# Performance work log

Hardware: AMD Instinct MI355X
Metric: run time of the kernel (lower is better)

The kernel has to match this reference:

```python
import jax, jax.numpy as jnp
import numpy as np

N_USERS = 100000
N_ITEMS = 50000
DIM = 64
HID = 64
E = 3200000
B = 16384


def setup_inputs() -> dict:
    key = jax.random.key(0)
    ks = jax.random.split(key, 16)
    N = N_USERS + N_ITEMS
    return {
        "users": jax.random.randint(ks[0], (B,), 0, N_USERS),
        "items": jax.random.randint(ks[1], (B,), 0, N_ITEMS),
        "edge_index": jax.random.randint(ks[2], (2, E), 0, N),
        "edge_weight": jax.random.uniform(ks[3], (E,), dtype=jnp.float32),
        # learned parameters
        "U": jax.random.normal(ks[4], (N_USERS, DIM), jnp.float32) * 0.1,
        "I": jax.random.normal(ks[5], (N_ITEMS, DIM), jnp.float32) * 0.1,
        "W0": jax.random.normal(ks[6], (DIM, HID), jnp.float32) / np.sqrt(DIM),
        "b0": jnp.zeros((HID,), jnp.float32),
        "g0": jnp.ones((HID,), jnp.float32),
        "be0": jnp.zeros((HID,), jnp.float32),
        "W1": jax.random.normal(ks[7], (HID, HID), jnp.float32) / np.sqrt(HID),
        "b1": jnp.zeros((HID,), jnp.float32),
        "g1": jnp.ones((HID,), jnp.float32),
        "be1": jnp.zeros((HID,), jnp.float32),
        "Wp": jax.random.normal(ks[8], (HID, DIM), jnp.float32) / np.sqrt(HID),
        "bp": jnp.zeros((DIM,), jnp.float32),
        "bu": jnp.zeros((N_USERS,), jnp.float32),
        "bi": jnp.zeros((N_ITEMS,), jnp.float32),
        "mu": jnp.zeros((), jnp.float32),
    }


def _layernorm(h, g, b, eps=1e-5):
    m = jnp.mean(h, axis=-1, keepdims=True)
    v = jnp.mean(jnp.square(h - m), axis=-1, keepdims=True)
    return (h - m) * jax.lax.rsqrt(v + eps) * g + b


def reference(users, items, edge_index, edge_weight, U, I,
              W0, b0, g0, be0, W1, b1, g1, be1, Wp, bp, bu, bi, mu):
    N = U.shape[0] + I.shape[0]
    x = jnp.concatenate([U, I], axis=0)  # [N, DIM]

    # GCN normalization with added self-loops (torch_geometric gcn_norm)
    loop = jnp.arange(N)
    src = jnp.concatenate([edge_index[0], loop])
    dst = jnp.concatenate([edge_index[1], loop])
    ew = jnp.concatenate([edge_weight, jnp.ones((N,), edge_weight.dtype)])
    deg = jax.ops.segment_sum(ew, dst, num_segments=N)
    dinv = jnp.where(deg > 0, jax.lax.rsqrt(deg), 0.0)
    norm = dinv[src] * ew * dinv[dst]  # [E+N]

    def conv(h, W, b):
        hw = h @ W  # [N, HID]
        msgs = norm[:, None] * hw[src]  # gather: [E+N, HID]
        return jax.ops.segment_sum(msgs, dst, num_segments=N) + b

    # layer 0: conv -> layernorm -> relu -> (dropout=identity, eval) -> residual
    h = x
    h_in = h
    h = conv(h, W0, b0)
    h = jax.nn.relu(_layernorm(h, g0, be0)) + h_in
    # layer 1
    h_in = h
    h = conv(h, W1, b1)
    h = jax.nn.relu(_layernorm(h, g1, be1)) + h_in

    h = h @ Wp + bp  # proj_out: [N, DIM]
    h_user = h[:U.shape[0]]
    h_item = h[U.shape[0]:]

    s = jnp.sum(h_user[users] * h_item[items], axis=-1)
    s = s + bu[users] + bi[items] + mu
    return jnp.clip(s, 1.0, 5.0)
```

## Files before the change

### kernel.cpp

```cpp
#include <hip/hip_runtime.h>

#define NU 100000
#define NI 50000
#define NN 150000
#define D  64
#define CAP 47
#define OVF_MAX 4096

#define BINSHIFT 8
#define BINW 256
#define NBINS 586
#define BINCAP 5848
#define STAGE_CAP 12
#define EPT 4
#define SPILL_CAP 262144
#define BIN_BLOCKS 768
#define GEMM_BLOCKS 2048

typedef unsigned int uint;
typedef unsigned short ushort;

__device__ __forceinline__ float half_reduce_add(float v) {
    #pragma unroll
    for (int m = 16; m >= 1; m >>= 1) v += __shfl_xor(v, m, 64);
    return v;
}
__device__ __forceinline__ ushort f2bf(float f) {
    union { float f; uint i; } c; c.f = f;
    uint r = c.i + 0x7FFF + ((c.i >> 16) & 1);
    return (ushort)(r >> 16);
}
__device__ __forceinline__ float lane_bcast(float v, int l) {
    return __int_as_float(__builtin_amdgcn_readlane(__float_as_int(v), l));
}
__device__ __forceinline__ uint enc14(float w) {
    uint b = __float_as_uint(w) + 0x00020000u;
    return b & 0xFFFC0000u;
}
__device__ __forceinline__ float dec14(uint r) {
    return __uint_as_float(r & 0xFFFC0000u);
}
__device__ __forceinline__ void spill_one(int d, uint s, float w,
        uint2* __restrict__ spill, int* __restrict__ spillcnt) {
    int si = atomicAdd(spillcnt, 1);
    if (si < SPILL_CAP) spill[si] = make_uint2(s | enc14(w), (uint)d);
}

__global__ __launch_bounds__(256) void k_bin_gemm(
        const int* __restrict__ src, const int* __restrict__ dst,
        const float* __restrict__ ew, int* __restrict__ bincur,
        uint2* __restrict__ binbuf, uint2* __restrict__ spill,
        int* __restrict__ spillcnt, int E,
        const float* __restrict__ U, const float* __restrict__ I,
        const float* __restrict__ W0, ushort* __restrict__ hw2b) {
    __shared__ uint2 stage[NBINS][STAGE_CAP];
    __shared__ int scnt[NBINS];
    if (blockIdx.x >= BIN_BLOCKS) {
        int lane = threadIdx.x & 63;
        float wreg[64];
        #pragma unroll
        for (int k = 0; k < 64; ++k) wreg[k] = W0[k * 64 + lane];
        int wid = (blockIdx.x - BIN_BLOCKS) * 4 + (threadIdx.x >> 6);
        int tw = GEMM_BLOCKS * 4;
        for (int n = wid; n < NN; n += tw) {
            float xv = (n < NU) ? U[(size_t)n * D + lane]
                                : I[(size_t)(n - NU) * D + lane];
            float a0 = 0.f, a1 = 0.f, a2 = 0.f, a3 = 0.f;
            #pragma unroll
            for (int k = 0; k < 64; k += 4) {
                a0 = fmaf(lane_bcast(xv, k + 0), wreg[k + 0], a0);
                a1 = fmaf(lane_bcast(xv, k + 1), wreg[k + 1], a1);
                a2 = fmaf(lane_bcast(xv, k + 2), wreg[k + 2], a2);
                a3 = fmaf(lane_bcast(xv, k + 3), wreg[k + 3], a3);
            }
            hw2b[(size_t)n * D + lane] = f2bf((a0 + a1) + (a2 + a3));
        }
        return;
    }
    int t = threadIdx.x;
    for (int i = t; i < NBINS; i += 256) scnt[i] = 0;
    __syncthreads();
    const int batch = 256 * EPT;
    for (int base = blockIdx.x * batch; base < E; base += BIN_BLOCKS * batch) {
        int dd[EPT]; uint ss[EPT]; float ww[EPT]; int ok[EPT];
        #pragma unroll
        for (int k = 0; k < EPT; ++k) {
            int e = base + k * 256 + t;
            ok[k] = (e < E);
            if (ok[k]) { dd[k] = dst[e]; ss[k] = (uint)src[e]; ww[k] = ew[e]; }
        }
        #pragma unroll
        for (int k = 0; k < EPT; ++k) {
            if (!ok[k]) continue;
            int bin = dd[k] >> BINSHIFT;
            int slot = atomicAdd(&scnt[bin], 1);
            if (slot < STAGE_CAP) {
                stage[bin][slot] = make_uint2(
                    ss[k] | ((uint)(dd[k] & (BINW - 1)) << 18),
                    (uint)__float_as_int(ww[k]));
            } else {
                spill_one(dd[k], ss[k], ww[k], spill, spillcnt);
            }
        }
        __syncthreads();
        for (int bin = t; bin < NBINS; bin += 256) {
            int c = scnt[bin]; if (c > STAGE_CAP) c = STAGE_CAP;
            while (c >= 8) {
                int b0 = atomicAdd(&bincur[bin], 8);
                if (b0 + 8 <= BINCAP) {
                    uint4* o4 = (uint4*)(binbuf + (size_t)bin * BINCAP + b0);
                    uint2* s2 = &stage[bin][c - 8];
                    o4[0] = make_uint4(s2[0].x, s2[0].y, s2[1].x, s2[1].y);
                    o4[1] = make_uint4(s2[2].x, s2[2].y, s2[3].x, s2[3].y);
                    o4[2] = make_uint4(s2[4].x, s2[4].y, s2[5].x, s2[5].y);
                    o4[3] = make_uint4(s2[6].x, s2[6].y, s2[7].x, s2[7].y);
                } else {
                    for (int j = 0; j < 8; ++j) {
                        uint2 r = stage[bin][c - 8 + j];
                        spill_one((bin << BINSHIFT) + (int)(r.x >> 18),
                                  r.x & 0x3FFFFu, __int_as_float((int)r.y),
                                  spill, spillcnt);
                    }
                }
                c -= 8;
            }
            scnt[bin] = c;
        }
        __syncthreads();
    }
    for (int bin = t; bin < NBINS; bin += 256) {
        int c = scnt[bin]; if (c > STAGE_CAP) c = STAGE_CAP;
        if (c > 0) {
            int b0 = atomicAdd(&bincur[bin], c);
            for (int j = 0; j < c; ++j) {
                uint2 r = stage[bin][j];
                if (b0 + j < BINCAP) binbuf[(size_t)bin * BINCAP + b0 + j] = r;
                else spill_one((bin << BINSHIFT) + (int)(r.x >> 18),
                               r.x & 0x3FFFFu, __int_as_float((int)r.y),
                               spill, spillcnt);
            }
        }
    }
}

__global__ __launch_bounds__(256) void k_regroup(
        const int* __restrict__ bincur, const uint2* __restrict__ binbuf,
        const uint2* __restrict__ spill, const int* __restrict__ spillcnt,
        uint* __restrict__ recs, int* __restrict__ cursor,
        float* __restrict__ dinv, int4* __restrict__ ovf,
        int* __restrict__ ovfcnt, ushort* __restrict__ hw2b) {
    __shared__ uint image[256 * CAP];
    __shared__ int cnt[256];
    __shared__ float ovfw[256];
    int t = threadIdx.x;
    int bin = blockIdx.x;
    cnt[t] = 0; ovfw[t] = 0.0f;
    __syncthreads();
    int dbase = bin << BINSHIFT;
    int nrec = bincur[bin]; if (nrec > BINCAP) nrec = BINCAP;
    const uint2* bb = binbuf + (size_t)bin * BINCAP;
    for (int i = t; i < nrec; i += 256) {
        uint2 r = bb[i];
        int dl = (int)(r.x >> 18);
        int slot = atomicAdd(&cnt[dl], 1);
        uint s = r.x & 0x3FFFFu;
        float w = __int_as_float((int)r.y);
        if (slot < CAP) image[dl * CAP + slot] = enc14(w) | s;
        else {
            atomicAdd(&ovfw[dl], w);
            int o = atomicAdd(ovfcnt, 1);
            if (o < OVF_MAX)
                ovf[o] = make_int4(dbase + dl, (int)s, __float_as_int(w), 0);
        }
    }
    int ns = spillcnt[0]; if (ns > SPILL_CAP) ns = SPILL_CAP;
    for (int i = t; i < ns; i += 256) {
        uint2 e = spill[i];
        int d = (int)e.y;
        if (d < dbase || d >= dbase + BINW) continue;
        int dl = d - dbase;
        int slot = atomicAdd(&cnt[dl], 1);
        if (slot < CAP) image[dl * CAP + slot] = e.x;
        else {
            float w = dec14(e.x);
            atomicAdd(&ovfw[dl], w);
            int o = atomicAdd(ovfcnt, 1);
            if (o < OVF_MAX) ovf[o] = make_int4(d, (int)(e.x & 0x3FFFFu),
                                                __float_as_int(w), 0);
        }
    }
    __syncthreads();
    int ndl = NN - dbase; if (ndl > 256) ndl = 256;
    if (ndl <= 0) return;
    if (t < ndl) {
        int c = cnt[t];
        cursor[dbase + t] = c;
        if (c > CAP) c = CAP;
        float dg = ovfw[t];
        for (int j = 0; j < c; ++j) dg += dec14(image[t * CAP + j]);
        float dv = rsqrtf(dg + 1.0f);
        dinv[dbase + t] = dv;
        ovfw[t] = dv;
    }
    int tot = ndl * CAP;
    uint* out = recs + (size_t)dbase * CAP;
    for (int i = t; i < tot; i += 256) out[i] = image[i];
    __syncthreads();
    uint* hw = (uint*)hw2b + (size_t)dbase * 32;
    int tot32 = ndl * 32;
    for (int i = t; i < tot32; i += 256) {
        float di = ovfw[i >> 5];
        uint v = hw[i];
        uint lo = (uint)f2bf(__uint_as_float(v << 16) * di);
        uint hi = (uint)f2bf(__uint_as_float(v & 0xFFFF0000u) * di);
        hw[i] = lo | (hi << 16);
    }
}

__device__ __forceinline__ float2 conv_accum2(int n, int lane,
        const uint* __restrict__ hw2p, const int* __restrict__ cursor,
        const uint* __restrict__ recs, const int4* __restrict__ ovf,
        const int* __restrict__ ovfcnt) {
    int cnt = __builtin_amdgcn_readfirstlane(cursor[n]);
    if (cnt > CAP) cnt = CAP;
    uint rv = (lane < cnt) ? recs[(size_t)n * CAP + lane] : 0u;
    const int  vodd4 = (lane >> 5) << 2;
    const uint lb4   = (uint)(lane & 31) << 2;
    uint xs = *(const uint*)((const char*)hw2p + (((uint)n << 7) + lb4));
    float ax = 0.f, ay = 0.f;
    int cp = (cnt + 7) & ~7;

#define CA_DECL(c) uint x##c##0, x##c##1, x##c##2, x##c##3, \
                        w##c##0, w##c##1, w##c##2, w##c##3;
#define CA_GET(c, i, P) { \
    uint r = (uint)__builtin_amdgcn_ds_bpermute(vodd4 + 8 * (P), (int)rv); \
    w##c##i = r & 0xFFFC0000u; \
    x##c##i = *(const uint*)((const char*)hw2p + \
                             (((r & 0x3FFFFu) << 7) + lb4)); }
#define CA_ISSUE(c, P0) { CA_GET(c, 0, (P0)+0) CA_GET(c, 1, (P0)+1) \
                          CA_GET(c, 2, (P0)+2) CA_GET(c, 3, (P0)+3) }
#define CA_FMA1(c, i) { \
    ax = fmaf(__uint_as_float(w##c##i), __uint_as_float(x##c##i << 16), ax); \
    ay = fmaf(__uint_as_float(w##c##i), \
              __uint_as_float(x##c##i & 0xFFFF0000u), ay); }
#define CA_FMA(c) { CA_FMA1(c,0) CA_FMA1(c,1) CA_FMA1(c,2) CA_FMA1(c,3) }

    CA_DECL(A) CA_DECL(B) CA_DECL(G)
    if (cp > 0)  CA_ISSUE(A, 0)
    if (cp > 8)  CA_ISSUE(B, 4)
    if (cp > 16) CA_ISSUE(G, 8)
    if (cp > 0)  CA_FMA(A)
    if (cp > 24) CA_ISSUE(A, 12)
    if (cp > 8)  CA_FMA(B)
    if (cp > 32) CA_ISSUE(B, 16)
    if (cp > 16) CA_FMA(G)
    if (cp > 40) CA_ISSUE(G, 20)
    if (cp > 24) CA_FMA(A)
    if (cp > 32) CA_FMA(B)
    if (cp > 40) CA_FMA(G)
#undef CA_FMA
#undef CA_FMA1
#undef CA_ISSUE
#undef CA_GET
#undef CA_DECL

    ax += __shfl_xor(ax, 32, 64);
    ay += __shfl_xor(ay, 32, 64);
    ax += __uint_as_float(xs << 16);
    ay += __uint_as_float(xs & 0xFFFF0000u);
    int novf = __builtin_amdgcn_readfirstlane(ovfcnt[0]);
    if (novf > 0) {
        if (novf > OVF_MAX) novf = OVF_MAX;
        for (int j = 0; j < novf; ++j) {
            int4 e = ovf[j];
            if (e.x == n) {
                float w = __int_as_float(e.z);
                uint x = hw2p[(size_t)e.y * 32 + (lane & 31)];
                ax = fmaf(w, __int_as_float((int)(x << 16)), ax);
                ay = fmaf(w, __int_as_float((int)(x & 0xFFFF0000u)), ay);
            }
        }
    }
    return make_float2(ax, ay);
}

__device__ __forceinline__ float2 ln_relu2(float2 a, float di, int p,
        const float* __restrict__ b, const float* __restrict__ g,
        const float* __restrict__ be) {
    float2 bb = ((const float2*)b)[p];
    float v0 = fmaf(a.x, di, bb.x);
    float v1 = fmaf(a.y, di, bb.y);
    float m = half_reduce_add(v0 + v1) * (1.0f / 64.0f);
    float d0 = v0 - m, d1 = v1 - m;
    float var = half_reduce_add(d0 * d0 + d1 * d1) * (1.0f / 64.0f);
    float rs = rsqrtf(var + 1e-5f);
    float2 gg = ((const float2*)g)[p];
    float2 ee = ((const float2*)be)[p];
    return make_float2(fmaxf(fmaf(d0 * rs, gg.x, ee.x), 0.0f),
                       fmaxf(fmaf(d1 * rs, gg.y, ee.y), 0.0f));
}

__global__ __launch_bounds__(256) void k_conv1(
        const uint* __restrict__ hw2p, const int* __restrict__ cursor,
        const uint* __restrict__ recs, const int4* __restrict__ ovf,
        const int* __restrict__ ovfcnt, const float* __restrict__ dinv,
        const float* __restrict__ b, const float* __restrict__ g,
        const float* __restrict__ be, const float* __restrict__ U,
        const float* __restrict__ I, uint* __restrict__ out1) {
    int lane = threadIdx.x & 63;
    int n = __builtin_amdgcn_readfirstlane(blockIdx.x * 4 + (threadIdx.x >> 6));
    if (n >= NN) return;
    float2 a = conv_accum2(n, lane, hw2p, cursor, recs, ovf, ovfcnt);
    int p = lane & 31;
    float2 y = ln_relu2(a, dinv[n], p, b, g, be);
    const float* R = (n < NU) ? (U + (size_t)n * D) : (I + (size_t)(n - NU) * D);
    float2 rr = ((const float2*)R)[p];
    if (lane < 32) {
        out1[(size_t)n * 32 + p] =
            (uint)f2bf(y.x + rr.x) | ((uint)f2bf(y.y + rr.y) << 16);
    }
}

__global__ __launch_bounds__(256) void k_gemm2(
        const ushort* __restrict__ hb, const float* __restrict__ W,
        const float* __restrict__ dinv, ushort* __restrict__ out) {
    int lane = threadIdx.x & 63;
    float wreg[64];
    #pragma unroll
    for (int k = 0; k < 64; ++k) wreg[k] = W[k * 64 + lane];
    int wpb = blockDim.x >> 6;
    int wid = blockIdx.x * wpb + (threadIdx.x >> 6);
    int tw = gridDim.x * wpb;
    for (int n = wid; n < NN; n += tw) {
        float xv = __uint_as_float((uint)hb[(size_t)n * D + lane] << 16);
        float a0 = 0.f, a1 = 0.f, a2 = 0.f, a3 = 0.f;
        #pragma unroll
        for (int k = 0; k < 64; k += 4) {
            a0 = fmaf(lane_bcast(xv, k + 0), wreg[k + 0], a0);
            a1 = fmaf(lane_bcast(xv, k + 1), wreg[k + 1], a1);
            a2 = fmaf(lane_bcast(xv, k + 2), wreg[k + 2], a2);
            a3 = fmaf(lane_bcast(xv, k + 3), wreg[k + 3], a3);
        }
        out[(size_t)n * D + lane] = f2bf(((a0 + a1) + (a2 + a3)) * dinv[n]);
    }
}

__global__ __launch_bounds__(256) void k_conv2score(
        const uint* __restrict__ hw2p, const int* __restrict__ cursor,
        const uint* __restrict__ recs, const int4* __restrict__ ovf,
        const int* __restrict__ ovfcnt, const float* __restrict__ dinv,
        const float* __restrict__ b, const float* __restrict__ g,
        const float* __restrict__ be, const int* __restrict__ users,
        const int* __restrict__ items, const uint* __restrict__ h1b,
        const float* __restrict__ Wp, const float* __restrict__ bp,
        const float* __restrict__ bu, const float* __restrict__ bi,
        const float* __restrict__ mu, float* __restrict__ out, int B) {
    int lane = threadIdx.x & 63;
    float wreg[64];
    #pragma unroll
    for (int k = 0; k < 64; ++k) wreg[k] = Wp[k * 64 + lane];
    float bpl = bp[lane];
    int q = lane & 31;
    int wpb = blockDim.x >> 6;
    int wid = blockIdx.x * wpb + (threadIdx.x >> 6);
    int tw = gridDim.x * wpb;
    for (int p = wid; p < B; p += tw) {
        int un = users[p];
        int in = NU + items[p];
        int nu = __builtin_amdgcn_readfirstlane(un);
        float2 au = conv_accum2(nu, lane, hw2p, cursor, recs, ovf, ovfcnt);
        float2 yu = ln_relu2(au, dinv[nu], q, b, g, be);
        uint xu = h1b[(size_t)nu * 32 + q];
        float2 hu = make_float2(yu.x + __uint_as_float(xu << 16),
                                yu.y + __uint_as_float(xu & 0xFFFF0000u));
        int ni = __builtin_amdgcn_readfirstlane(in);
        float2 ai = conv_accum2(ni, lane, hw2p, cursor, recs, ovf, ovfcnt);
        float2 yi = ln_relu2(ai, dinv[ni], q, b, g, be);
        uint xi = h1b[(size_t)ni * 32 + q];
        float2 hi = make_float2(yi.x + __uint_as_float(xi << 16),
                                yi.y + __uint_as_float(xi & 0xFFFF0000u));
        float pu = bpl, pi = bpl;
        #pragma unroll
        for (int j = 0; j < 32; ++j) {
            pu = fmaf(lane_bcast(hu.x, j), wreg[2 * j], pu);
            pu = fmaf(lane_bcast(hu.y, j), wreg[2 * j + 1], pu);
            pi = fmaf(lane_bcast(hi.x, j), wreg[2 * j], pi);
            pi = fmaf(lane_bcast(hi.y, j), wreg[2 * j + 1], pi);
        }
        float t = pu * pi;
        #pragma unroll
        for (int m = 32; m >= 1; m >>= 1) t += __shfl_xor(t, m, 64);
        if (lane == 0) {
            t += bu[un] + bi[in - NU] + mu[0];
            out[p] = fminf(fmaxf(t, 1.0f), 5.0f);
        }
    }
}

extern "C" void kernel_launch(void* const* d_in, const int* in_sizes, int n_in,
                              void* d_out, int out_size, void* d_ws, size_t ws_size,
                              hipStream_t stream) {
    const int*   users = (const int*)d_in[0];
    const int*   items = (const int*)d_in[1];
    const int*   ei2   = (const int*)d_in[2];
    const float* ew    = (const float*)d_in[3];
    const float* U     = (const float*)d_in[4];
    const float* I     = (const float*)d_in[5];
    const float* W0    = (const float*)d_in[6];
    const float* b0    = (const float*)d_in[7];
    const float* g0    = (const float*)d_in[8];
    const float* be0   = (const float*)d_in[9];
    const float* W1    = (const float*)d_in[10];
    const float* b1    = (const float*)d_in[11];
    const float* g1    = (const float*)d_in[12];
    const float* be1   = (const float*)d_in[13];
    const float* Wp    = (const float*)d_in[14];
    const float* bp    = (const float*)d_in[15];
    const float* bu    = (const float*)d_in[16];
    const float* bi    = (const float*)d_in[17];
    const float* mu    = (const float*)d_in[18];

    int B = in_sizes[0];
    int E = in_sizes[2] / 2;
    const int* srcp = ei2;
    const int* dstp = ei2 + E;

    char* p = (char*)d_ws;
    auto alloc = [&](size_t bytes) -> char* {
        char* r = p;
        p += (bytes + 255) & ~(size_t)255;
        return r;
    };
    int*    cbuf    = (int*)  alloc((size_t)(NBINS + 8) * 4);
    int*    bincur  = cbuf;
    int*    spillcnt= cbuf + NBINS;
    int*    ovfcnt  = cbuf + NBINS + 1;
    int*    cursor  = (int*)  alloc((size_t)NN * 4);
    float*  dinv    = (float*)alloc((size_t)NN * 4);
    int4*   ovf     = (int4*) alloc((size_t)OVF_MAX * 16);
    uint2*  spill   = (uint2*)alloc((size_t)SPILL_CAP * 8);
    uint2*  binbuf  = (uint2*)alloc((size_t)NBINS * BINCAP * 8);
    uint*   recs    = (uint*) alloc((size_t)NN * CAP * 4);
    ushort* hw2b    = (ushort*)alloc((size_t)NN * D * 2);
    uint*   h1b     = (uint*) alloc((size_t)NN * 32 * 4);
    const uint* hw2p = (const uint*)hw2b;

    hipMemsetAsync(cbuf, 0, (size_t)(NBINS + 8) * 4, stream);

    int gW = (NN + 3) / 4;

    k_bin_gemm<<<BIN_BLOCKS + GEMM_BLOCKS, 256, 0, stream>>>(
        srcp, dstp, ew, bincur, binbuf, spill, spillcnt, E, U, I, W0, hw2b);
    k_regroup<<<NBINS, 256, 0, stream>>>(bincur, binbuf, spill, spillcnt,
                                         recs, cursor, dinv, ovf, ovfcnt, hw2b);

    k_conv1<<<gW, 256, 0, stream>>>(hw2p, cursor, recs, ovf, ovfcnt, dinv,
                                    b0, g0, be0, U, I, h1b);
    k_gemm2<<<2048, 256, 0, stream>>>((const ushort*)h1b, W1, dinv, hw2b);
    k_conv2score<<<1024, 256, 0, stream>>>(hw2p, cursor, recs, ovf, ovfcnt, dinv,
                                           b1, g1, be1, users, items, h1b,
                                           Wp, bp, bu, bi, mu,
                                           (float*)d_out, B);
}
```

Baseline: 430.8 us.

## Split layer-0 GEMM out of binning kernel and fold dinv scaling into it

The first-layer X@W0 GEMM no longer runs as extra blocks inside the edge-binning kernel. It now runs as a separate kernel after regroup, which lets it multiply by dinv before the bf16 store. This removes regroup's read-modify-write pass that rescaled hw2b, and avoids rounding to bf16 twice. The cost is that the GEMM can no longer overlap with binning, an extra launch is added, and the binning stage capacity is reduced slightly.

```diff
diff --git a/kernel.cpp b/kernel.cpp
--- a/kernel.cpp
+++ b/kernel.cpp
@@ -11,11 +11,10 @@
 #define BINW 256
 #define NBINS 586
 #define BINCAP 5848
-#define STAGE_CAP 12
+#define STAGE_CAP 11
 #define EPT 4
 #define SPILL_CAP 262144
 #define BIN_BLOCKS 768
-#define GEMM_BLOCKS 2048
 
 typedef unsigned int uint;
 typedef unsigned short ushort;
@@ -46,37 +45,13 @@
     if (si < SPILL_CAP) spill[si] = make_uint2(s | enc14(w), (uint)d);
 }
 
-__global__ __launch_bounds__(256) void k_bin_gemm(
+__global__ __launch_bounds__(256) void k_bin(
         const int* __restrict__ src, const int* __restrict__ dst,
         const float* __restrict__ ew, int* __restrict__ bincur,
         uint2* __restrict__ binbuf, uint2* __restrict__ spill,
-        int* __restrict__ spillcnt, int E,
-        const float* __restrict__ U, const float* __restrict__ I,
-        const float* __restrict__ W0, ushort* __restrict__ hw2b) {
+        int* __restrict__ spillcnt, int E) {
     __shared__ uint2 stage[NBINS][STAGE_CAP];
     __shared__ int scnt[NBINS];
-    if (blockIdx.x >= BIN_BLOCKS) {
-        int lane = threadIdx.x & 63;
-        float wreg[64];
-        #pragma unroll
-        for (int k = 0; k < 64; ++k) wreg[k] = W0[k * 64 + lane];
-        int wid = (blockIdx.x - BIN_BLOCKS) * 4 + (threadIdx.x >> 6);
-        int tw = GEMM_BLOCKS * 4;
-        for (int n = wid; n < NN; n += tw) {
-            float xv = (n < NU) ? U[(size_t)n * D + lane]
-                                : I[(size_t)(n - NU) * D + lane];
-            float a0 = 0.f, a1 = 0.f, a2 = 0.f, a3 = 0.f;
-            #pragma unroll
-            for (int k = 0; k < 64; k += 4) {
-                a0 = fmaf(lane_bcast(xv, k + 0), wreg[k + 0], a0);
-                a1 = fmaf(lane_bcast(xv, k + 1), wreg[k + 1], a1);
-                a2 = fmaf(lane_bcast(xv, k + 2), wreg[k + 2], a2);
-                a3 = fmaf(lane_bcast(xv, k + 3), wreg[k + 3], a3);
-            }
-            hw2b[(size_t)n * D + lane] = f2bf((a0 + a1) + (a2 + a3));
-        }
-        return;
-    }
     int t = threadIdx.x;
     for (int i = t; i < NBINS; i += 256) scnt[i] = 0;
     __syncthreads();
@@ -148,7 +123,7 @@
         const uint2* __restrict__ spill, const int* __restrict__ spillcnt,
         uint* __restrict__ recs, int* __restrict__ cursor,
         float* __restrict__ dinv, int4* __restrict__ ovf,
-        int* __restrict__ ovfcnt, ushort* __restrict__ hw2b) {
+        int* __restrict__ ovfcnt) {
     __shared__ uint image[256 * CAP];
     __shared__ int cnt[256];
     __shared__ float ovfw[256];
@@ -198,22 +173,36 @@
         if (c > CAP) c = CAP;
         float dg = ovfw[t];
         for (int j = 0; j < c; ++j) dg += dec14(image[t * CAP + j]);
-        float dv = rsqrtf(dg + 1.0f);
-        dinv[dbase + t] = dv;
-        ovfw[t] = dv;
+        dinv[dbase + t] = rsqrtf(dg + 1.0f);
     }
     int tot = ndl * CAP;
     uint* out = recs + (size_t)dbase * CAP;
     for (int i = t; i < tot; i += 256) out[i] = image[i];
-    __syncthreads();
-    uint* hw = (uint*)hw2b + (size_t)dbase * 32;
-    int tot32 = ndl * 32;
-    for (int i = t; i < tot32; i += 256) {
-        float di = ovfw[i >> 5];
-        uint v = hw[i];
-        uint lo = (uint)f2bf(__uint_as_float(v << 16) * di);
-        uint hi = (uint)f2bf(__uint_as_float(v & 0xFFFF0000u) * di);
-        hw[i] = lo | (hi << 16);
+}
+
+__global__ __launch_bounds__(256) void k_gemm1(
+        const float* __restrict__ U, const float* __restrict__ I,
+        const float* __restrict__ W, const float* __restrict__ dinv,
+        ushort* __restrict__ out) {
+    int lane = threadIdx.x & 63;
+    float wreg[64];
+    #pragma unroll
+    for (int k = 0; k < 64; ++k) wreg[k] = W[k * 64 + lane];
+    int wpb = blockDim.x >> 6;
+    int wid = blockIdx.x * wpb + (threadIdx.x >> 6);
+    int tw = gridDim.x * wpb;
+    for (int n = wid; n < NN; n += tw) {
+        float xv = (n < NU) ? U[(size_t)n * D + lane]
+                            : I[(size_t)(n - NU) * D + lane];
+        float a0 = 0.f, a1 = 0.f, a2 = 0.f, a3 = 0.f;
+        #pragma unroll
+        for (int k = 0; k < 64; k += 4) {
+            a0 = fmaf(lane_bcast(xv, k + 0), wreg[k + 0], a0);
+            a1 = fmaf(lane_bcast(xv, k + 1), wreg[k + 1], a1);
+            a2 = fmaf(lane_bcast(xv, k + 2), wreg[k + 2], a2);
+            a3 = fmaf(lane_bcast(xv, k + 3), wreg[k + 3], a3);
+        }
+        out[(size_t)n * D + lane] = f2bf(((a0 + a1) + (a2 + a3)) * dinv[n]);
     }
 }
 
@@ -449,11 +438,12 @@
 
     int gW = (NN + 3) / 4;
 
-    k_bin_gemm<<<BIN_BLOCKS + GEMM_BLOCKS, 256, 0, stream>>>(
-        srcp, dstp, ew, bincur, binbuf, spill, spillcnt, E, U, I, W0, hw2b);
+    k_bin<<<BIN_BLOCKS, 256, 0, stream>>>(srcp, dstp, ew, bincur, binbuf,
+                                          spill, spillcnt, E);
     k_regroup<<<NBINS, 256, 0, stream>>>(bincur, binbuf, spill, spillcnt,
-                                         recs, cursor, dinv, ovf, ovfcnt, hw2b);
-
+                                         recs, cursor, dinv, ovf, ovfcnt);
+
+    k_gemm1<<<2048, 256, 0, stream>>>(U, I, W0, dinv, hw2b);
     k_conv1<<<gW, 256, 0, stream>>>(hw2p, cursor, recs, ovf, ovfcnt, dinv,
                                     b0, g0, be0, U, I, h1b);
     k_gemm2<<<2048, 256, 0, stream>>>((const ushort*)h1b, W1, dinv, hw2b);
```

Result: no change. 437.3 us (+1.5%).
